# Kernel tuning notes

Hardware: AMD Instinct MI355X
Metric: run time of the kernel (lower is better)

## Reference

```python
import jax, jax.numpy as jnp
import numpy as np


def setup_inputs() -> dict:
    key = jax.random.key(0)
    ks = jax.random.split(key, 10)
    B, L, D_MODEL = 2, 2048, 1024
    D_INNER, N, W, R = 2048, 16, 4, 64
    s = 0.02
    return {
        "hidden_states": jax.random.normal(ks[0], (B, L, D_MODEL), jnp.float32),
        "in_proj_w": jax.random.normal(ks[1], (2 * D_INNER, D_MODEL), jnp.float32) * s,
        "conv_w": jax.random.normal(ks[2], (D_INNER, W), jnp.float32) * 0.2,
        "conv_b": jax.random.normal(ks[3], (D_INNER,), jnp.float32) * 0.02,
        "x_proj_w": jax.random.normal(ks[4], (R + 2 * N, D_INNER), jnp.float32) * s,
        "dt_proj_w": jax.random.normal(ks[5], (D_INNER, R), jnp.float32) * (R ** -0.5),
        "dt_proj_b": jnp.log(jnp.expm1(jnp.exp(jax.random.uniform(ks[6], (D_INNER,), jnp.float32, np.log(1e-3), np.log(1e-1)))) + 1e-20),
        "A_log": jnp.log(jnp.broadcast_to(jnp.arange(1, N + 1, dtype=jnp.float32), (D_INNER, N))),
        "D_param": jnp.ones((D_INNER,), jnp.float32),
        "out_proj_w": jax.random.normal(ks[7], (D_MODEL, D_INNER), jnp.float32) * s,
    }


def _mamba_fwd(hidden_states, in_proj_w, conv_w, conv_b, x_proj_w,
               dt_proj_w, dt_proj_b, A_log, D_param, out_proj_w):
    Bsz, L, _ = hidden_states.shape
    d_inner = conv_w.shape[0]
    n = A_log.shape[1]
    r = dt_proj_w.shape[1]

    # input projection -> x, z  (each [B, L, d_inner])
    xz = jnp.einsum('bld,ed->ble', hidden_states, in_proj_w)
    x, z = xz[..., :d_inner], xz[..., d_inner:]

    # depthwise causal conv over L with SiLU
    x_bdl = jnp.transpose(x, (0, 2, 1))  # [B, d, L]
    kern = conv_w[:, None, :]            # [d, 1, W]
    xc = jax.lax.conv_general_dilated(
        x_bdl, kern, window_strides=(1,), padding=[(conv_w.shape[1] - 1, 0)],
        dimension_numbers=('NCH', 'OIH', 'NCH'), feature_group_count=d_inner)
    xc = xc + conv_b[None, :, None]
    xc = xc * jax.nn.sigmoid(xc)         # silu, [B, d, L]
    u = jnp.transpose(xc, (0, 2, 1))     # [B, L, d]

    # SSM parameter projections
    x_dbl = jnp.einsum('bld,ed->ble', u, x_proj_w)   # [B, L, r+2n]
    dt_lo = x_dbl[..., :r]
    B_ssm = x_dbl[..., r:r + n]                       # [B, L, n]
    C_ssm = x_dbl[..., r + n:]                        # [B, L, n]
    delta = jax.nn.softplus(jnp.einsum('blr,dr->bld', dt_lo, dt_proj_w) + dt_proj_b)

    A = -jnp.exp(A_log)  # [d, n]

    # selective scan over time (sequential recurrence)
    def step(h, inp):
        d_t, u_t, b_t, c_t = inp  # [B,d], [B,d], [B,n], [B,n]
        dA = jnp.exp(d_t[..., None] * A)                       # [B,d,n]
        h = dA * h + (d_t * u_t)[..., None] * b_t[:, None, :]  # [B,d,n]
        y_t = jnp.einsum('bdn,bn->bd', h, c_t)
        return h, y_t

    h0 = jnp.zeros((Bsz, d_inner, n), dtype=u.dtype)
    xs = (jnp.transpose(delta, (1, 0, 2)), jnp.transpose(u, (1, 0, 2)),
          jnp.transpose(B_ssm, (1, 0, 2)), jnp.transpose(C_ssm, (1, 0, 2)))
    _, ys = jax.lax.scan(step, h0, xs)           # ys: [L, B, d]
    y = jnp.transpose(ys, (1, 0, 2)) + u * D_param
    y = y * (z * jax.nn.sigmoid(z))              # gate: y * silu(z)
    return jnp.einsum('bld,ed->ble', y, out_proj_w)


def reference(hidden_states, in_proj_w, conv_w, conv_b, x_proj_w,
              dt_proj_w, dt_proj_b, A_log, D_param, out_proj_w):
    return _mamba_fwd(hidden_states, in_proj_w, conv_w, conv_b, x_proj_w,
                      dt_proj_w, dt_proj_b, A_log, D_param, out_proj_w)
```

## Files before the change

### kernel.cpp

```cpp
#include <hip/hip_runtime.h>
#include <cstdint>
#include <cstddef>

#define Bsz  2
#define Lseq 2048
#define DM   1024
#define DI   2048
#define NS   16
#define RR   64
#define BL   (Bsz * Lseq)
#define TC   64
#define NC   (Lseq / TC)

typedef unsigned short u16;
typedef __attribute__((ext_vector_type(4))) unsigned short u16x4;
typedef __attribute__((ext_vector_type(8))) short short8;
typedef __attribute__((ext_vector_type(4))) float f32x4;

__device__ __forceinline__ u16 f32_to_bf16(float f) {
  union { float f; unsigned int u; } v; v.f = f;
  unsigned int lsb = (v.u >> 16) & 1u;
  v.u += 0x7fffu + lsb;
  return (u16)(v.u >> 16);
}
__device__ __forceinline__ float bf16_to_f32(u16 h) {
  union { unsigned int u; float f; } v; v.u = ((unsigned int)h) << 16;
  return v.f;
}

#define N0 (BL * DM)
#define N1 (2 * DI * DM)
#define N2 (96 * DI)
#define N3 (DM * DI)
#define N4 (DI * 64)
__global__ __launch_bounds__(256) void cvt_fused(
    const float* __restrict__ hs, u16* __restrict__ hs_b,
    const float* __restrict__ win, u16* __restrict__ win_b,
    const float* __restrict__ wxp, u16* __restrict__ wxp_b,
    const float* __restrict__ wout, u16* __restrict__ wout_b,
    const float* __restrict__ wdt, u16* __restrict__ w_hi, u16* __restrict__ w_lo)
{
  int i = (blockIdx.x * blockDim.x + threadIdx.x) * 4;
  const float* src; u16* dst;
  if (i < N0)                     { src = hs;   dst = hs_b; }
  else if ((i -= N0) < N1)        { src = win;  dst = win_b; }
  else if ((i -= N1) < N2)        { src = wxp;  dst = wxp_b; }
  else if ((i -= N2) < N3)        { src = wout; dst = wout_b; }
  else if ((i -= N3) < N4) {
    const float4 v = *(const float4*)(wdt + i);
#pragma unroll
    for (int j = 0; j < 4; ++j) {
      const float f = ((const float*)&v)[j];
      const u16 h = f32_to_bf16(f);
      w_hi[i + j] = h;
      w_lo[i + j] = f32_to_bf16(f - bf16_to_f32(h));
    }
    return;
  } else return;
  const float4 v = *(const float4*)(src + i);
  dst[i + 0] = f32_to_bf16(v.x);
  dst[i + 1] = f32_to_bf16(v.y);
  dst[i + 2] = f32_to_bf16(v.z);
  dst[i + 3] = f32_to_bf16(v.w);
}
#define CVT_TOTAL (N0 + N1 + N2 + N3 + N4)

__device__ __forceinline__ void gload_lds16(const u16* g, u16* l) {
  __builtin_amdgcn_global_load_lds(
      (const __attribute__((address_space(1))) unsigned int*)g,
      (__attribute__((address_space(3))) unsigned int*)l,
      16, 0, 0);
}

__global__ __launch_bounds__(256) void gemm128_bt(
    const u16* __restrict__ A, const u16* __restrict__ Bt,
    float* __restrict__ outA, float* __restrict__ outB,
    int split, int ldA, int ldB, int K, int kstride, size_t zstride)
{
  __shared__ __align__(16) u16 As[128 * 32];
  __shared__ __align__(16) u16 Bs[128 * 32];
  const int tid  = threadIdx.x;
  const int lane = tid & 63;
  const int wid  = tid >> 6;
  const int m0 = blockIdx.y * 128;
  const int n0 = blockIdx.x * 128;
  const int kbase = blockIdx.z * K;
  const int wr = wid >> 1, wc = wid & 1;

  const f32x4 zero = {0.f, 0.f, 0.f, 0.f};
  f32x4 acc[4][4];
#pragma unroll
  for (int i = 0; i < 4; ++i)
#pragma unroll
    for (int j = 0; j < 4; ++j) acc[i][j] = zero;

  const int l16 = lane * 16;

  for (int k0 = 0; k0 < K; k0 += 32) {
    __syncthreads();
#pragma unroll
    for (int c = 0; c < 2; ++c) {
      const int base = c * 4096 + wid * 1024;
      const int ofs  = base + l16;
      const int row  = ofs >> 6;
      const int col  = (ofs >> 1) & 31;
      gload_lds16(A  + (size_t)(m0 + row) * kstride + kbase + k0 + col, (u16*)((char*)As + base));
      gload_lds16(Bt + (size_t)(n0 + row) * kstride + kbase + k0 + col, (u16*)((char*)Bs + base));
    }
    __syncthreads();

    const int kk = (lane >> 4) * 8;
    const int ra = wr * 64 + (lane & 15);
    const int rb = wc * 64 + (lane & 15);
    short8 af[4], bf[4];
#pragma unroll
    for (int i = 0; i < 4; ++i) af[i] = *(const short8*)&As[(ra + i * 16) * 32 + kk];
#pragma unroll
    for (int j = 0; j < 4; ++j) bf[j] = *(const short8*)&Bs[(rb + j * 16) * 32 + kk];
#pragma unroll
    for (int i = 0; i < 4; ++i)
#pragma unroll
      for (int j = 0; j < 4; ++j)
        acc[i][j] = __builtin_amdgcn_mfma_f32_16x16x32_bf16(af[i], bf[j], acc[i][j], 0, 0, 0);
  }

  const int cr = (lane >> 4) * 4;
  const int cc = lane & 15;
#pragma unroll
  for (int i = 0; i < 4; ++i)
#pragma unroll
    for (int j = 0; j < 4; ++j)
#pragma unroll
      for (int r = 0; r < 4; ++r) {
        const int m = m0 + wr * 64 + i * 16 + cr + r;
        const int n = n0 + wc * 64 + j * 16 + cc;
        const float v = acc[i][j][r];
        if (n < split) outA[(size_t)m * ldA + n + blockIdx.z * zstride] = v;
        else           outB[(size_t)m * ldB + (n - split)] = v;
      }
}

__global__ void add2_kernel(const float* __restrict__ part, float* __restrict__ out) {
  const int i = (blockIdx.x * blockDim.x + threadIdx.x) * 4;
  const float4 a = *(const float4*)(part + i);
  const float4 b = *(const float4*)(part + (size_t)BL * DM + i);
  float4 s;
  s.x = a.x + b.x; s.y = a.y + b.y; s.z = a.z + b.z; s.w = a.w + b.w;
  *(float4*)(out + i) = s;
}

__global__ __launch_bounds__(256) void gemm_xproj(
    const u16* __restrict__ A, const u16* __restrict__ Bt,
    float* __restrict__ xdbl, u16* __restrict__ dhi, u16* __restrict__ dlo)
{
  const int wg   = blockIdx.x * 4 + (threadIdx.x >> 6);
  const int lane = threadIdx.x & 63;
  const int mt = wg / 6, nt = wg % 6;

  const u16* arow = A  + (size_t)(mt * 16 + (lane & 15)) * DI + ((lane >> 4) * 8);
  const u16* brow = Bt + (size_t)(nt * 16 + (lane & 15)) * DI + ((lane >> 4) * 8);
  f32x4 acc = {0.f, 0.f, 0.f, 0.f};
  for (int k0 = 0; k0 < DI; k0 += 32) {
    short8 a = *(const short8*)(arow + k0);
    short8 b = *(const short8*)(brow + k0);
    acc = __builtin_amdgcn_mfma_f32_16x16x32_bf16(a, b, acc, 0, 0, 0);
  }
  const int cr = (lane >> 4) * 4, cc = lane & 15;
  const int n  = nt * 16 + cc;
#pragma unroll
  for (int r = 0; r < 4; ++r) {
    const int m = mt * 16 + cr + r;
    const float v = acc[r];
    if (n < RR) {
      const u16 h = f32_to_bf16(v);
      dhi[(size_t)m * RR + n] = h;
      dlo[(size_t)m * RR + n] = f32_to_bf16(v - bf16_to_f32(h));
    } else {
      xdbl[(size_t)m * 96 + n] = v;
    }
  }
}

__global__ __launch_bounds__(256) void dt_gemm_mfma(
    const u16* __restrict__ ahi, const u16* __restrict__ alo,
    const u16* __restrict__ bhi, const u16* __restrict__ blo,
    const float* __restrict__ dtb, float* __restrict__ delta)
{
  const int wg   = blockIdx.x * 4 + (threadIdx.x >> 6);
  const int lane = threadIdx.x & 63;
  const int mt = wg >> 7, nt = wg & 127;

  const size_t aofs = (size_t)(mt * 16 + (lane & 15)) * 64 + ((lane >> 4) * 8);
  const size_t bofs = (size_t)(nt * 16 + (lane & 15)) * 64 + ((lane >> 4) * 8);

  f32x4 acc = {0.f, 0.f, 0.f, 0.f};
#pragma unroll
  for (int k0 = 0; k0 < 64; k0 += 32) {
    const short8 Ah = *(const short8*)(ahi + aofs + k0);
    const short8 Al = *(const short8*)(alo + aofs + k0);
    const short8 Bh = *(const short8*)(bhi + bofs + k0);
    const short8 Bl = *(const short8*)(blo + bofs + k0);
    acc = __builtin_amdgcn_mfma_f32_16x16x32_bf16(Ah, Bh, acc, 0, 0, 0);
    acc = __builtin_amdgcn_mfma_f32_16x16x32_bf16(Ah, Bl, acc, 0, 0, 0);
    acc = __builtin_amdgcn_mfma_f32_16x16x32_bf16(Al, Bh, acc, 0, 0, 0);
  }

  const int cr = (lane >> 4) * 4, cc = lane & 15;
  const int n  = nt * 16 + cc;
  const float b = dtb[n];
#pragma unroll
  for (int r = 0; r < 4; ++r) {
    const float s = acc[r] + b;
    const float sp = fmaxf(s, 0.f) + __logf(1.f + __expf(-fabsf(s)));
    delta[(size_t)(mt * 16 + cr + r) * DI + n] = sp;
  }
}

__global__ __launch_bounds__(256) void conv_silu_kernel(
    const float* __restrict__ x,
    const float* __restrict__ cw, const float* __restrict__ cb,
    u16* __restrict__ ub)
{
  const int idx  = blockIdx.x * blockDim.x + threadIdx.x;
  const int base = idx * 4;
  const int d  = base & (DI - 1);
  const int bl = base >> 11;
  const int l  = bl & (Lseq - 1);
  const float* xp = x + (size_t)bl * DI + d;
  const float4 zf = {0.f, 0.f, 0.f, 0.f};
  const float4 x3 = *(const float4*)xp;
  const float4 x2 = (l >= 1) ? *(const float4*)(xp - DI)     : zf;
  const float4 x1 = (l >= 2) ? *(const float4*)(xp - 2 * DI) : zf;
  const float4 x0 = (l >= 3) ? *(const float4*)(xp - 3 * DI) : zf;
  const float4 bias = *(const float4*)&cb[d];
  u16x4 out;
#pragma unroll
  for (int j = 0; j < 4; ++j) {
    const float4 w = *(const float4*)&cw[(d + j) * 4];
    float acc = ((const float*)&bias)[j];
    acc += ((const float*)&x0)[j] * w.x + ((const float*)&x1)[j] * w.y +
           ((const float*)&x2)[j] * w.z + ((const float*)&x3)[j] * w.w;
    const float s = acc / (1.f + __expf(-acc));
    out[j] = f32_to_bf16(s);
  }
  *(u16x4*)(ub + (size_t)bl * DI + d) = out;
}


__global__ __launch_bounds__(256) void scan_chunk_ps(
    const float* __restrict__ delta, const u16* __restrict__ u,
    const float* __restrict__ xdbl, const float* __restrict__ alog,
    float* __restrict__ Pout, float* __restrict__ Sout)
{
  __shared__ float Bl[TC][NS];
  const int b   = blockIdx.z;
  const int c   = blockIdx.y;
  const int d   = blockIdx.x * 256 + threadIdx.x;
  const int tid = threadIdx.x;
  const size_t rowBase = (size_t)b * Lseq + (size_t)c * TC;

  {
    const int row = tid >> 2, c4 = (tid & 3) * 4;
    *(float4*)&Bl[row][c4] = *(const float4*)&xdbl[(rowBase + row) * 96 + RR + c4];
  }
  __syncthreads();

  float A[NS];
#pragma unroll
  for (int n4 = 0; n4 < 4; ++n4) {
    const float4 a4 = *(const float4*)&alog[(size_t)d * NS + n4 * 4];
    A[n4 * 4 + 0] = -__expf(a4.x);
    A[n4 * 4 + 1] = -__expf(a4.y);
    A[n4 * 4 + 2] = -__expf(a4.z);
    A[n4 * 4 + 3] = -__expf(a4.w);
  }

  float h[NS], P[NS];
#pragma unroll
  for (int n = 0; n < NS; ++n) { h[n] = 0.f; P[n] = 1.f; }

#pragma unroll 4
  for (int t = 0; t < TC; ++t) {
    const float dt  = delta[(rowBase + t) * DI + d];
    const float ut  = bf16_to_f32(u[(rowBase + t) * DI + d]);
    const float dtu = dt * ut;
#pragma unroll
    for (int n = 0; n < NS; ++n) {
      const float dA = __expf(dt * A[n]);
      P[n] *= dA;
      h[n] = dA * h[n] + dtu * Bl[t][n];
    }
  }

  const size_t base = (size_t)(b * NC + c) * NS * DI + d;
#pragma unroll
  for (int n = 0; n < NS; ++n) {
    Pout[base + (size_t)n * DI] = P[n];
    Sout[base + (size_t)n * DI] = h[n];
  }
}

__global__ __launch_bounds__(256) void scan_combine(
    const float* __restrict__ P, const float* __restrict__ S,
    float* __restrict__ Hin)
{
  const int gid = blockIdx.x * 256 + threadIdx.x;
  const int b   = gid >> 15;
  const int nd  = gid & 32767;
  float h = 0.f;
  for (int c = 0; c < NC; ++c) {
    const size_t o = (size_t)(b * NC + c) * (NS * DI) + nd;
    const float Pc = P[o];
    const float Sc = S[o];
    Hin[o] = h;
    h = Pc * h + Sc;
  }
}

__global__ __launch_bounds__(256) void scan_chunk_y(
    const float* __restrict__ delta, const u16* __restrict__ u,
    const float* __restrict__ xdbl, const float* __restrict__ alog,
    const float* __restrict__ dpar, const float* __restrict__ z,
    const float* __restrict__ Hin, u16* __restrict__ yb)
{
  __shared__ float Bl[TC][NS];
  __shared__ float Cl[TC][NS];
  const int b   = blockIdx.z;
  const int c   = blockIdx.y;
  const int d   = blockIdx.x * 256 + threadIdx.x;
  const int tid = threadIdx.x;
  const size_t rowBase = (size_t)b * Lseq + (size_t)c * TC;

  {
    const int row = tid >> 2, c4 = (tid & 3) * 4;
    *(float4*)&Bl[row][c4] = *(const float4*)&xdbl[(rowBase + row) * 96 + RR + c4];
    *(float4*)&Cl[row][c4] = *(const float4*)&xdbl[(rowBase + row) * 96 + RR + NS + c4];
  }
  __syncthreads();

  float A[NS];
#pragma unroll
  for (int n4 = 0; n4 < 4; ++n4) {
    const float4 a4 = *(const float4*)&alog[(size_t)d * NS + n4 * 4];
    A[n4 * 4 + 0] = -__expf(a4.x);
    A[n4 * 4 + 1] = -__expf(a4.y);
    A[n4 * 4 + 2] = -__expf(a4.z);
    A[n4 * 4 + 3] = -__expf(a4.w);
  }
  const float Dv = dpar[d];

  float h[NS];
  const size_t sbase = (size_t)(b * NC + c) * NS * DI + d;
#pragma unroll
  for (int n = 0; n < NS; ++n) h[n] = Hin[sbase + (size_t)n * DI];

#pragma unroll 4
  for (int t = 0; t < TC; ++t) {
    const float dt  = delta[(rowBase + t) * DI + d];
    const float ut  = bf16_to_f32(u[(rowBase + t) * DI + d]);
    const float zv  = z[(rowBase + t) * DI + d];
    const float dtu = dt * ut;
    float y = 0.f;
#pragma unroll
    for (int n = 0; n < NS; ++n) {
      const float dA = __expf(dt * A[n]);
      h[n] = dA * h[n] + dtu * Bl[t][n];
      y += h[n] * Cl[t][n];
    }
    const float yv = y + ut * Dv;
    const float g  = zv / (1.f + __expf(-zv));
    yb[(rowBase + t) * DI + d] = f32_to_bf16(yv * g);
  }
}

extern "C" void kernel_launch(void* const* d_in, const int* in_sizes, int n_in,
                              void* d_out, int out_size, void* d_ws, size_t ws_size,
                              hipStream_t stream)
{
  const float* hs   = (const float*)d_in[0];
  const float* win  = (const float*)d_in[1];
  const float* cw   = (const float*)d_in[2];
  const float* cb   = (const float*)d_in[3];
  const float* wxp  = (const float*)d_in[4];
  const float* wdt  = (const float*)d_in[5];
  const float* bdt  = (const float*)d_in[6];
  const float* alog = (const float*)d_in[7];
  const float* dpar = (const float*)d_in[8];
  const float* wout = (const float*)d_in[9];
  float* out = (float*)d_out;

  char* ws = (char*)d_ws;
  size_t off = 0;
  auto alloc = [&](size_t bytes) -> void* {
    void* p = ws + off;
    off += (bytes + 255) & ~(size_t)255;
    return p;
  };
  u16*   hs_b   = (u16*)  alloc((size_t)BL * DM * 2);
  u16*   win_b  = (u16*)  alloc((size_t)2 * DI * DM * 2);
  u16*   wxp_b  = (u16*)  alloc((size_t)96 * DI * 2);
  u16*   wout_b = (u16*)  alloc((size_t)DM * DI * 2);
  float* xbuf   = (float*)alloc((size_t)BL * DI * 4);
  float* zbuf   = (float*)alloc((size_t)BL * DI * 4);
  u16*   ub16   = (u16*)  alloc((size_t)BL * DI * 2);
  float* deltab = (float*)alloc((size_t)BL * DI * 4);
  float* xdbl   = (float*)alloc((size_t)BL * 96 * 4);
  float* Pbuf   = (float*)alloc((size_t)Bsz * NC * DI * NS * 4);
  float* Sbuf   = (float*)alloc((size_t)Bsz * NC * DI * NS * 4);
  u16*   dt_hi  = (u16*)  alloc((size_t)BL * 64 * 2);
  u16*   dt_lo  = (u16*)  alloc((size_t)BL * 64 * 2);
  u16*   w_hi   = (u16*)  alloc((size_t)DI * 64 * 2);
  u16*   w_lo   = (u16*)  alloc((size_t)DI * 64 * 2);
  u16*   y_b    = ub16;
  float* Hin    = Pbuf;
  float* part   = deltab;

  cvt_fused<<<(CVT_TOTAL / 4 + 255) / 256, 256, 0, stream>>>(
      hs, hs_b, win, win_b, wxp, wxp_b, wout, wout_b, wdt, w_hi, w_lo);

  {
    dim3 g(4096 / 128, BL / 128);
    gemm128_bt<<<g, 256, 0, stream>>>(hs_b, win_b, xbuf, zbuf,
                                      DI, DI, DI, DM, DM, 0);
  }

  conv_silu_kernel<<<(BL * DI / 4) / 256, 256, 0, stream>>>(xbuf, cw, cb, ub16);

  gemm_xproj<<<(256 * 6) / 4, 256, 0, stream>>>(ub16, wxp_b, xdbl, dt_hi, dt_lo);

  dt_gemm_mfma<<<(256 * 128) / 4, 256, 0, stream>>>(dt_hi, dt_lo, w_hi, w_lo, bdt, deltab);

  {
    dim3 gA(DI / 256, NC, Bsz);
    scan_chunk_ps<<<gA, 256, 0, stream>>>(deltab, ub16, xdbl, alog, Pbuf, Sbuf);
    scan_combine<<<(Bsz * DI * NS) / 256, 256, 0, stream>>>(Pbuf, Sbuf, Hin);
    scan_chunk_y<<<gA, 256, 0, stream>>>(deltab, ub16, xdbl, alog, dpar, zbuf, Hin, y_b);
  }

  {
    dim3 g(DM / 128, BL / 128, 2);
    gemm128_bt<<<g, 256, 0, stream>>>(y_b, wout_b, part, part,
                                      1 << 30, DM, DM, DI / 2, DI,
                                      (size_t)BL * DM);
    add2_kernel<<<(BL * DM / 4) / 256, 256, 0, stream>>>(part, out);
  }
}
```

Before: 296.3 us.

## Fuse dt projection and softplus into both scan kernels via LDS

```diff
diff --git a/kernel.cpp b/kernel.cpp
--- a/kernel.cpp
+++ b/kernel.cpp
@@ -178,41 +178,6 @@
     } else {
       xdbl[(size_t)m * 96 + n] = v;
     }
-  }
-}
-
-__global__ __launch_bounds__(256) void dt_gemm_mfma(
-    const u16* __restrict__ ahi, const u16* __restrict__ alo,
-    const u16* __restrict__ bhi, const u16* __restrict__ blo,
-    const float* __restrict__ dtb, float* __restrict__ delta)
-{
-  const int wg   = blockIdx.x * 4 + (threadIdx.x >> 6);
-  const int lane = threadIdx.x & 63;
-  const int mt = wg >> 7, nt = wg & 127;
-
-  const size_t aofs = (size_t)(mt * 16 + (lane & 15)) * 64 + ((lane >> 4) * 8);
-  const size_t bofs = (size_t)(nt * 16 + (lane & 15)) * 64 + ((lane >> 4) * 8);
-
-  f32x4 acc = {0.f, 0.f, 0.f, 0.f};
-#pragma unroll
-  for (int k0 = 0; k0 < 64; k0 += 32) {
-    const short8 Ah = *(const short8*)(ahi + aofs + k0);
-    const short8 Al = *(const short8*)(alo + aofs + k0);
-    const short8 Bh = *(const short8*)(bhi + bofs + k0);
-    const short8 Bl = *(const short8*)(blo + bofs + k0);
-    acc = __builtin_amdgcn_mfma_f32_16x16x32_bf16(Ah, Bh, acc, 0, 0, 0);
-    acc = __builtin_amdgcn_mfma_f32_16x16x32_bf16(Ah, Bl, acc, 0, 0, 0);
-    acc = __builtin_amdgcn_mfma_f32_16x16x32_bf16(Al, Bh, acc, 0, 0, 0);
-  }
-
-  const int cr = (lane >> 4) * 4, cc = lane & 15;
-  const int n  = nt * 16 + cc;
-  const float b = dtb[n];
-#pragma unroll
-  for (int r = 0; r < 4; ++r) {
-    const float s = acc[r] + b;
-    const float sp = fmaxf(s, 0.f) + __logf(1.f + __expf(-fabsf(s)));
-    delta[(size_t)(mt * 16 + cr + r) * DI + n] = sp;
   }
 }
 
@@ -247,22 +212,66 @@
 }
 
 
-__global__ __launch_bounds__(256) void scan_chunk_ps(
-    const float* __restrict__ delta, const u16* __restrict__ u,
+__device__ __forceinline__ void compute_delta_lds(
+    float (*dl)[256],
+    const u16* __restrict__ dhi, const u16* __restrict__ dlo,
+    const u16* __restrict__ whi, const u16* __restrict__ wlo,
+    const float* __restrict__ dtb, int d0, size_t rowBase)
+{
+  const int tid  = threadIdx.x;
+  const int lane = tid & 63;
+  const int rt   = tid >> 6;
+  const size_t arow = (rowBase + rt * 16 + (lane & 15)) * RR + ((lane >> 4) * 8);
+  const short8 Ah0 = *(const short8*)(dhi + arow);
+  const short8 Ah1 = *(const short8*)(dhi + arow + 32);
+  const short8 Al0 = *(const short8*)(dlo + arow);
+  const short8 Al1 = *(const short8*)(dlo + arow + 32);
+  const int cr = (lane >> 4) * 4, cc = lane & 15;
+#pragma unroll 4
+  for (int ct = 0; ct < 16; ++ct) {
+    const size_t brow = (size_t)(d0 + ct * 16 + (lane & 15)) * RR + ((lane >> 4) * 8);
+    const short8 Bh0 = *(const short8*)(whi + brow);
+    const short8 Bh1 = *(const short8*)(whi + brow + 32);
+    const short8 Bl0 = *(const short8*)(wlo + brow);
+    const short8 Bl1 = *(const short8*)(wlo + brow + 32);
+    f32x4 acc = {0.f, 0.f, 0.f, 0.f};
+    acc = __builtin_amdgcn_mfma_f32_16x16x32_bf16(Ah0, Bh0, acc, 0, 0, 0);
+    acc = __builtin_amdgcn_mfma_f32_16x16x32_bf16(Ah0, Bl0, acc, 0, 0, 0);
+    acc = __builtin_amdgcn_mfma_f32_16x16x32_bf16(Al0, Bh0, acc, 0, 0, 0);
+    acc = __builtin_amdgcn_mfma_f32_16x16x32_bf16(Ah1, Bh1, acc, 0, 0, 0);
+    acc = __builtin_amdgcn_mfma_f32_16x16x32_bf16(Ah1, Bl1, acc, 0, 0, 0);
+    acc = __builtin_amdgcn_mfma_f32_16x16x32_bf16(Al1, Bh1, acc, 0, 0, 0);
+    const float b = dtb[d0 + ct * 16 + cc];
+#pragma unroll
+    for (int r = 0; r < 4; ++r) {
+      const float s  = acc[r] + b;
+      const float sp = fmaxf(s, 0.f) + __logf(1.f + __expf(-fabsf(s)));
+      dl[rt * 16 + cr + r][ct * 16 + cc] = sp;
+    }
+  }
+}
+
+__global__ __launch_bounds__(256) void scan_ps_fused(
+    const u16* __restrict__ dhi, const u16* __restrict__ dlo,
+    const u16* __restrict__ whi, const u16* __restrict__ wlo,
+    const float* __restrict__ dtb, const u16* __restrict__ u,
     const float* __restrict__ xdbl, const float* __restrict__ alog,
     float* __restrict__ Pout, float* __restrict__ Sout)
 {
+  __shared__ float dl[TC][256];
   __shared__ float Bl[TC][NS];
   const int b   = blockIdx.z;
   const int c   = blockIdx.y;
-  const int d   = blockIdx.x * 256 + threadIdx.x;
+  const int d0  = blockIdx.x * 256;
   const int tid = threadIdx.x;
+  const int d   = d0 + tid;
   const size_t rowBase = (size_t)b * Lseq + (size_t)c * TC;
 
   {
     const int row = tid >> 2, c4 = (tid & 3) * 4;
     *(float4*)&Bl[row][c4] = *(const float4*)&xdbl[(rowBase + row) * 96 + RR + c4];
   }
+  compute_delta_lds(dl, dhi, dlo, whi, wlo, dtb, d0, rowBase);
   __syncthreads();
 
   float A[NS];
@@ -281,7 +290,7 @@
 
 #pragma unroll 4
   for (int t = 0; t < TC; ++t) {
-    const float dt  = delta[(rowBase + t) * DI + d];
+    const float dt  = dl[t][tid];
     const float ut  = bf16_to_f32(u[(rowBase + t) * DI + d]);
     const float dtu = dt * ut;
 #pragma unroll
@@ -317,18 +326,22 @@
   }
 }
 
-__global__ __launch_bounds__(256) void scan_chunk_y(
-    const float* __restrict__ delta, const u16* __restrict__ u,
+__global__ __launch_bounds__(256) void scan_y_fused(
+    const u16* __restrict__ dhi, const u16* __restrict__ dlo,
+    const u16* __restrict__ whi, const u16* __restrict__ wlo,
+    const float* __restrict__ dtb, const u16* __restrict__ u,
     const float* __restrict__ xdbl, const float* __restrict__ alog,
     const float* __restrict__ dpar, const float* __restrict__ z,
     const float* __restrict__ Hin, u16* __restrict__ yb)
 {
+  __shared__ float dl[TC][256];
   __shared__ float Bl[TC][NS];
   __shared__ float Cl[TC][NS];
   const int b   = blockIdx.z;
   const int c   = blockIdx.y;
-  const int d   = blockIdx.x * 256 + threadIdx.x;
+  const int d0  = blockIdx.x * 256;
   const int tid = threadIdx.x;
+  const int d   = d0 + tid;
   const size_t rowBase = (size_t)b * Lseq + (size_t)c * TC;
 
   {
@@ -336,6 +349,7 @@
     *(float4*)&Bl[row][c4] = *(const float4*)&xdbl[(rowBase + row) * 96 + RR + c4];
     *(float4*)&Cl[row][c4] = *(const float4*)&xdbl[(rowBase + row) * 96 + RR + NS + c4];
   }
+  compute_delta_lds(dl, dhi, dlo, whi, wlo, dtb, d0, rowBase);
   __syncthreads();
 
   float A[NS];
@@ -356,7 +370,7 @@
 
 #pragma unroll 4
   for (int t = 0; t < TC; ++t) {
-    const float dt  = delta[(rowBase + t) * DI + d];
+    const float dt  = dl[t][tid];
     const float ut  = bf16_to_f32(u[(rowBase + t) * DI + d]);
     const float zv  = z[(rowBase + t) * DI + d];
     const float dtu = dt * ut;
@@ -403,7 +417,7 @@
   float* xbuf   = (float*)alloc((size_t)BL * DI * 4);
   float* zbuf   = (float*)alloc((size_t)BL * DI * 4);
   u16*   ub16   = (u16*)  alloc((size_t)BL * DI * 2);
-  float* deltab = (float*)alloc((size_t)BL * DI * 4);
+  float* part   = (float*)alloc((size_t)2 * BL * DM * 4);
   float* xdbl   = (float*)alloc((size_t)BL * 96 * 4);
   float* Pbuf   = (float*)alloc((size_t)Bsz * NC * DI * NS * 4);
   float* Sbuf   = (float*)alloc((size_t)Bsz * NC * DI * NS * 4);
@@ -413,7 +427,6 @@
   u16*   w_lo   = (u16*)  alloc((size_t)DI * 64 * 2);
   u16*   y_b    = ub16;
   float* Hin    = Pbuf;
-  float* part   = deltab;
 
   cvt_fused<<<(CVT_TOTAL / 4 + 255) / 256, 256, 0, stream>>>(
       hs, hs_b, win, win_b, wxp, wxp_b, wout, wout_b, wdt, w_hi, w_lo);
@@ -428,13 +441,13 @@
 
   gemm_xproj<<<(256 * 6) / 4, 256, 0, stream>>>(ub16, wxp_b, xdbl, dt_hi, dt_lo);
 
-  dt_gemm_mfma<<<(256 * 128) / 4, 256, 0, stream>>>(dt_hi, dt_lo, w_hi, w_lo, bdt, deltab);
-
   {
     dim3 gA(DI / 256, NC, Bsz);
-    scan_chunk_ps<<<gA, 256, 0, stream>>>(deltab, ub16, xdbl, alog, Pbuf, Sbuf);
+    scan_ps_fused<<<gA, 256, 0, stream>>>(dt_hi, dt_lo, w_hi, w_lo, bdt,
+                                          ub16, xdbl, alog, Pbuf, Sbuf);
     scan_combine<<<(Bsz * DI * NS) / 256, 256, 0, stream>>>(Pbuf, Sbuf, Hin);
-    scan_chunk_y<<<gA, 256, 0, stream>>>(deltab, ub16, xdbl, alog, dpar, zbuf, Hin, y_b);
+    scan_y_fused<<<gA, 256, 0, stream>>>(dt_hi, dt_lo, w_hi, w_lo, bdt,
+                                         ub16, xdbl, alog, dpar, zbuf, Hin, y_b);
   }
 
   {
```

New measurement: 290.3 us. 1.02x faster.
